# Kernel optimization log

Hardware: AMD Instinct MI355X
Metric: run time of the kernel (lower is better)

The kernel has to match this reference:

```python
import jax, jax.numpy as jnp
import numpy as np

B_SI = 4.1491   # neutron scattering length Si (fm)
B_O = 5.803     # neutron scattering length O (fm)
CUTOFF = 3.5    # tetrahedral neighbour cutoff (A)
BIG = 1e6       # masked-distance sentinel (finite to keep grads NaN-free)


def setup_inputs() -> dict:
    key = jax.random.key(0)
    k1, k2 = jax.random.split(key)
    N, L = 4096, 40.0
    positions = jax.random.uniform(k1, (N, 3), dtype=jnp.float32) * L
    cell = (L * jnp.eye(3)).astype(jnp.float32)
    r_bins = (0.05 + 0.05 * jnp.arange(200, dtype=jnp.float32))      # 0.05..10.0 A
    q_bins = jnp.linspace(0.5, 25.0, 500, dtype=jnp.float32)          # A^-1
    species = jax.random.randint(k2, (N,), 0, 3, dtype=jnp.int32)     # 0=Si, 1/2=O
    return {"positions": positions, "cell": cell, "r_bins": r_bins,
            "q_bins": q_bins, "species": species}


def _pair_geometry(positions, cell):
    # Minimum-image displacements under a general periodic cell.
    disp = positions[:, None, :] - positions[None, :, :]        # [N,N,3]
    frac = disp @ jnp.linalg.inv(cell)
    frac = frac - jnp.round(frac)
    disp = frac @ cell
    d2 = jnp.sum(disp * disp, axis=-1)                           # [N,N]
    self_mask = jnp.eye(positions.shape[0], dtype=bool)
    dist = jnp.sqrt(jnp.where(self_mask, 1.0, d2))               # safe sqrt on diag
    return disp, dist, self_mask


def reference(positions, cell, r_bins, q_bins, species):
    N = positions.shape[0]
    nbins = r_bins.shape[0]
    dtype = positions.dtype

    disp, dist, self_mask = _pair_geometry(positions, cell)

    # --- neutron-weighted G(r): differentiable linear (cloud-in-cell) binning ---
    b = jnp.where(species == 0, B_SI, B_O).astype(dtype)         # per-atom scattering length
    w = (b[:, None] * b[None, :]) / (jnp.mean(b) ** 2)           # Faber-Ziman pair weights
    r0, dr = r_bins[0], r_bins[1] - r_bins[0]
    x = (dist - r0) / dr
    i0 = jnp.floor(x).astype(jnp.int32)
    f = x - i0.astype(dtype)
    valid = (~self_mask) & (i0 >= 0) & (i0 < nbins - 1)
    w0 = jnp.where(valid, w * (1.0 - f), 0.0).ravel()
    w1 = jnp.where(valid, w * f, 0.0).ravel()
    i0f = jnp.clip(i0, 0, nbins - 1).ravel()
    hist = (jnp.zeros(nbins, dtype)
            .at[i0f].add(w0)
            .at[jnp.clip(i0f + 1, 0, nbins - 1)].add(w1))
    V = jnp.abs(jnp.linalg.det(cell))
    rho = N / V
    shell = 4.0 * jnp.pi * r_bins ** 2 * dr                       # ideal-gas shell volume
    G_r = hist / (N * rho * shell)                                # [nbins]

    # --- total correlation function T(r) = 4 pi rho r G(r) ---
    T_r = 4.0 * jnp.pi * rho * r_bins * G_r

    # --- structure factor S(Q) = 1 + 4 pi rho int r^2 (G(r)-1) sinc(Qr) dr ---
    qr = q_bins[:, None] * r_bins[None, :]                        # [nQ, nr]
    integrand = (r_bins ** 2) * (G_r - 1.0)
    S_Q = 1.0 + 4.0 * jnp.pi * rho * dr * jnp.sum(
        integrand[None, :] * jnp.sinc(qr / jnp.pi), axis=1)

    # --- tetrahedral order parameter q_tet over Si centres with O neighbours ---
    central = species == 0
    nbr_ok = (species != 0)[None, :] & (~self_mask)
    nd = jnp.where(nbr_ok, dist, BIG)
    negd, idx = jax.lax.top_k(-nd, 4)                             # 4 nearest O per atom
    d4 = -negd                                                    # [N,4]
    u = jnp.take_along_axis(disp, idx[:, :, None], axis=1) / d4[:, :, None]  # unit vecs
    cosang = jnp.einsum('nkd,nld->nkl', u, u)                     # [N,4,4]
    pair_mask = jnp.triu(jnp.ones((4, 4), bool), 1)               # 6 angle pairs
    q_i = 1.0 - (3.0 / 8.0) * jnp.sum(((cosang + 1.0 / 3.0) ** 2) * pair_mask, axis=(1, 2))
    vf = (central & (d4[:, 3] < CUTOFF)).astype(dtype)            # needs 4 nbrs in cutoff
    q_tet = jnp.sum(q_i * vf) / jnp.maximum(jnp.sum(vf), 1.0)

    return G_r, T_r, S_Q, q_tet
```

## Files before the change

kernel.cpp:

```cpp
#include <hip/hip_runtime.h>
#include <climits>
#include <math.h>


#define B_SI_F 4.1491f
#define B_O_F  5.803f
#define CUTOFF_F 3.5f
#define CS2 12.25350025f
#define NCOPIES 16
#define CAP 32

#define WS_HIST 16
#define WS_ACC  3328
#define WS_CNT  4096

__device__ __forceinline__ bool dless(float da, int ia, float db, int ib) {
    return (da < db) || (da == db && ia < ib);
}

struct CellK {
    float ci0, ci1, ci2, ci3, ci4, ci5, ci6, ci7, ci8;
    float c0, c1, c2, c3, c4, c5, c6, c7, c8;
};

__device__ __forceinline__ CellK make_cell(const float* __restrict__ cellm,
                                           bool& diag) {
    CellK K;
    K.c0 = cellm[0]; K.c1 = cellm[1]; K.c2 = cellm[2];
    K.c3 = cellm[3]; K.c4 = cellm[4]; K.c5 = cellm[5];
    K.c6 = cellm[6]; K.c7 = cellm[7]; K.c8 = cellm[8];
    double m0 = K.c0, m1 = K.c1, m2 = K.c2;
    double m3 = K.c3, m4 = K.c4, m5 = K.c5;
    double m6 = K.c6, m7 = K.c7, m8 = K.c8;
    double det = m0*(m4*m8 - m5*m7) - m1*(m3*m8 - m5*m6) + m2*(m3*m7 - m4*m6);
    double rd = 1.0 / det;
    K.ci0 = (float)( (m4*m8 - m5*m7) * rd);
    K.ci1 = (float)(-(m1*m8 - m2*m7) * rd);
    K.ci2 = (float)( (m1*m5 - m2*m4) * rd);
    K.ci3 = (float)(-(m3*m8 - m5*m6) * rd);
    K.ci4 = (float)( (m0*m8 - m2*m6) * rd);
    K.ci5 = (float)(-(m0*m5 - m2*m3) * rd);
    K.ci6 = (float)( (m3*m7 - m4*m6) * rd);
    K.ci7 = (float)(-(m0*m7 - m1*m6) * rd);
    K.ci8 = (float)( (m0*m4 - m1*m3) * rd);
    diag = (K.c1 == 0.0f) && (K.c2 == 0.0f) && (K.c3 == 0.0f) &&
           (K.c5 == 0.0f) && (K.c6 == 0.0f) && (K.c7 == 0.0f);
    return K;
}

template<bool DIAG>
__device__ __forceinline__ void min_image(const CellK& K,
                                          float dx, float dy, float dz,
                                          float& ex, float& ey, float& ez) {
    if (DIAG) {
        float t0 = dx * K.ci0, t1 = dy * K.ci4, t2 = dz * K.ci8;
        t0 -= rintf(t0);  t1 -= rintf(t1);  t2 -= rintf(t2);
        ex = t0 * K.c0;  ey = t1 * K.c4;  ez = t2 * K.c8;
    } else {
        float f0 = dx*K.ci0 + dy*K.ci3 + dz*K.ci6;
        float f1 = dx*K.ci1 + dy*K.ci4 + dz*K.ci7;
        float f2 = dx*K.ci2 + dy*K.ci5 + dz*K.ci8;
        f0 -= rintf(f0);  f1 -= rintf(f1);  f2 -= rintf(f2);
        ex = f0*K.c0 + f1*K.c3 + f2*K.c6;
        ey = f0*K.c1 + f1*K.c4 + f2*K.c7;
        ez = f0*K.c2 + f1*K.c5 + f2*K.c8;
    }
}

template<bool DIAG>
__device__ __forceinline__ void hist_sweep(const CellK& K,
                                           const float4* __restrict__ sj,
                                           const float4* __restrict__ sjc,
                                           int lbase, int jb0,
                                           float fi0, float fi1, float fi2,
                                           float xi, float yi, float zi,
                                           float wi, float inv_dr, float nrb0,
                                           int nbins_m1, float* shc,
                                           bool iSi, bool iO, bool offdiag, int iidx,
                                           float* __restrict__ cnt,
                                           float4* __restrict__ cand) {
    #pragma unroll 4
    for (int l = 0; l < 64; ++l) {
        const float4 pj = sj[lbase + l];
        float d0 = fi0 - pj.x;  d0 -= rintf(d0);
        float d1 = fi1 - pj.y;  d1 -= rintf(d1);
        float d2 = fi2 - pj.z;  d2 -= rintf(d2);
        float ex, ey, ez;
        if (DIAG) {
            ex = d0 * K.c0;  ey = d1 * K.c4;  ez = d2 * K.c8;
        } else {
            ex = d0*K.c0 + d1*K.c3 + d2*K.c6;
            ey = d0*K.c1 + d1*K.c4 + d2*K.c7;
            ez = d0*K.c2 + d1*K.c5 + d2*K.c8;
        }
        float dsq  = fmaf(ex, ex, fmaf(ey, ey, ez * ez));
        float dist = __builtin_amdgcn_sqrtf(dsq);
        float x  = fmaf(dist, inv_dr, nrb0);
        float fl = floorf(x);
        int   i0 = (int)fl;
        if ((unsigned)i0 < (unsigned)nbins_m1) {
            float w  = wi * pj.w;
            float wf = w * (x - fl);
            atomicAdd(&shc[i0],     w - wf);
            atomicAdd(&shc[i0 + 1], wf);
        }
        if (dsq < CS2) {
            const int jg = jb0 + lbase + l;
            if (iSi && pj.w == B_O_F) {
                float old = atomicAdd(&cnt[iidx], 1.0f);
                int slot = (int)rintf(old);
                if (slot < CAP) {
                    float4 cj = sjc[lbase + l];
                    cj.w = __int_as_float(jg);
                    cand[iidx * CAP + slot] = cj;
                }
            }
            if (offdiag && iO && pj.w == B_SI_F) {
                float old = atomicAdd(&cnt[jg], 1.0f);
                int slot = (int)rintf(old);
                if (slot < CAP)
                    cand[jg * CAP + slot] = make_float4(xi, yi, zi, __int_as_float(iidx));
            }
        }
    }
}

__global__ __launch_bounds__(256) void k_main(const float* __restrict__ cellm,
                                              const float* __restrict__ pos,
                                              const int* __restrict__ species,
                                              const float* __restrict__ rbins,
                                              float* __restrict__ ws,
                                              int N, int nbins, int T) {
    const int tid = threadIdx.x;
    const int bid = blockIdx.x;

    bool diag;
    const CellK K = make_cell(cellm, diag);

    __shared__ float sh[4 * 257];
    __shared__ float sjf[128 * 4];
    __shared__ float sjc[128 * 4];

    for (int u = tid; u < 4 * 257; u += 256) sh[u] = 0.0f;

    int rem = bid, ti = 0;
    while (rem >= T - ti) { rem -= T - ti; ti++; }
    const int tj  = ti + rem;
    const int jb0 = tj * 128;

    for (int u = tid; u < 384; u += 256) {
        int g = 3 * jb0 + u;
        sjc[(u / 3) * 4 + (u % 3)] = (g < 3 * N) ? pos[g] : 0.0f;
    }
    if (tid < 128) {
        int ja = jb0 + tid;
        sjf[tid * 4 + 3] = (ja < N) ? ((species[ja] == 0) ? B_SI_F : B_O_F) : 0.0f;
    }
    __syncthreads();
    if (tid < 128) {
        float x = sjc[tid*4], y = sjc[tid*4+1], z = sjc[tid*4+2];
        float f0, f1, f2;
        if (diag) { f0 = x*K.ci0; f1 = y*K.ci4; f2 = z*K.ci8; }
        else {
            f0 = x*K.ci0 + y*K.ci3 + z*K.ci6;
            f1 = x*K.ci1 + y*K.ci4 + z*K.ci7;
            f2 = x*K.ci2 + y*K.ci5 + z*K.ci8;
        }
        sjf[tid*4] = f0;  sjf[tid*4+1] = f1;  sjf[tid*4+2] = f2;
    }

    const float rb0      = rbins[0];
    const float inv_dr   = 1.0f / (rbins[1] - rbins[0]);
    const float nrb0     = -rb0 * inv_dr;
    const int   nbins_m1 = nbins - 1;

    const int il  = tid & 127;
    const int sub = tid >> 7;
    const int i   = ti * 128 + il;
    const int ig  = min(i, N - 1);
    const float xi = pos[3*ig], yi = pos[3*ig+1], zi = pos[3*ig+2];
    float fi0, fi1, fi2;
    if (diag) { fi0 = xi*K.ci0; fi1 = yi*K.ci4; fi2 = zi*K.ci8; }
    else {
        fi0 = xi*K.ci0 + yi*K.ci3 + zi*K.ci6;
        fi1 = xi*K.ci1 + yi*K.ci4 + zi*K.ci7;
        fi2 = xi*K.ci2 + yi*K.ci5 + zi*K.ci8;
    }
    const int   spi  = species[ig];
    const float b_i  = (spi == 0) ? B_SI_F : B_O_F;
    const float wmul = (ti == tj) ? 1.0f : 2.0f;
    const float wi   = (i < N) ? b_i * wmul : 0.0f;
    const bool iSi = (i < N) && (spi == 0);
    const bool iO  = (i < N) && (spi != 0);
    const bool offdiag = (ti != tj);

    float*  cnt  = ws + WS_CNT;
    float4* cand = (float4*)(ws + WS_CNT + (size_t)N);
    float*  shc  = sh + ((tid >> 4) & 3) * 257;

    __syncthreads();

    const float4* sj   = (const float4*)sjf;
    const float4* sjc4 = (const float4*)sjc;
    const int lbase = sub * 64;
    if (diag) hist_sweep<true >(K, sj, sjc4, lbase, jb0, fi0, fi1, fi2, xi, yi, zi, wi, inv_dr, nrb0, nbins_m1, shc, iSi, iO, offdiag, i, cnt, cand);
    else      hist_sweep<false>(K, sj, sjc4, lbase, jb0, fi0, fi1, fi2, xi, yi, zi, wi, inv_dr, nrb0, nbins_m1, shc, iSi, iO, offdiag, i, cnt, cand);

    __syncthreads();

    float* gh = ws + WS_HIST + (size_t)(bid % NCOPIES) * nbins;
    for (int t = tid; t < nbins; t += 256) {
        float h = sh[t] + sh[257 + t] + sh[514 + t] + sh[771 + t];
        if (h != 0.0f) atomicAdd(&gh[t], h);
    }
}

#define INS4D(c, jc, ex, ey, ez)                                           \
{                                                                          \
    if (dless(c, jc, e3, j3)) {                                            \
        bool lt2 = dless(c, jc, e2, j2);                                   \
        bool lt1 = dless(c, jc, e1, j1);                                   \
        bool lt0 = dless(c, jc, e0, j0);                                   \
        e3 = lt2 ? e2 : c;               j3 = lt2 ? j2 : jc;               \
        x3 = lt2 ? x2 : ex;  y3 = lt2 ? y2 : ey;  z3 = lt2 ? z2 : ez;      \
        e2 = lt2 ? (lt1 ? e1 : c) : e2;  j2 = lt2 ? (lt1 ? j1 : jc) : j2;  \
        x2 = lt2 ? (lt1 ? x1 : ex) : x2;                                   \
        y2 = lt2 ? (lt1 ? y1 : ey) : y2;                                   \
        z2 = lt2 ? (lt1 ? z1 : ez) : z2;                                   \
        e1 = lt1 ? (lt0 ? e0 : c) : e1;  j1 = lt1 ? (lt0 ? j0 : jc) : j1;  \
        x1 = lt1 ? (lt0 ? x0 : ex) : x1;                                   \
        y1 = lt1 ? (lt0 ? y0 : ey) : y1;                                   \
        z1 = lt1 ? (lt0 ? z0 : ez) : z1;                                   \
        e0 = lt0 ? c : e0;               j0 = lt0 ? jc : j0;               \
        x0 = lt0 ? ex : x0;  y0 = lt0 ? ey : y0;  z0 = lt0 ? ez : z0;      \
    }                                                                      \
}

__device__ __forceinline__ float fast_sinc(float x) {
    float rev = x * 0.15915494309189535f;
    rev -= rintf(rev);
    float sn = __builtin_amdgcn_sinf(rev);
    return sn * __builtin_amdgcn_rcpf(x);
}

__global__ __launch_bounds__(256) void k_fin(const float* __restrict__ cellm,
                                             float* __restrict__ ws,
                                             const float* __restrict__ rbins,
                                             const float* __restrict__ qbins,
                                             const int* __restrict__ species,
                                             const float* __restrict__ pos,
                                             float* __restrict__ out,
                                             int N, int nbins, int nq,
                                             int QB, int BT) {
    const int tid = threadIdx.x;
    const int bid = blockIdx.x;

    if (bid >= QB) {
        __shared__ float swq[4], swv[4];
        __shared__ float sacc[128];
        __shared__ int   slast;
        const int tb   = bid - QB;
        const int wid  = tid >> 6;
        const int lane = tid & 63;
        const int s = __builtin_amdgcn_readfirstlane(tb * 4 + wid);

        float* cnt = ws + WS_CNT;
        const float4* cand = (const float4*)(ws + WS_CNT + (size_t)N);

        float qiv = 0.0f, vf = 0.0f;
        if (s < N && species[s] == 0) {
            bool diag;
            const CellK K = make_cell(cellm, diag);
            const float xi = pos[3*s], yi = pos[3*s+1], zi = pos[3*s+2];
            const int c = (int)rintf(cnt[s]);
            if (lane == 0) cnt[s] = 0.0f;

            float e0 = 1e30f, e1 = 1e30f, e2 = 1e30f, e3 = 1e30f;
            int   j0 = INT_MAX, j1 = INT_MAX, j2 = INT_MAX, j3 = INT_MAX;
            float x0 = 0, y0 = 0, z0 = 0, x1 = 0, y1 = 0, z1 = 0;
            float x2 = 0, y2 = 0, z2 = 0, x3 = 0, y3 = 0, z3 = 0;

            if (c <= CAP) {
                if (lane < c) {
                    float4 cd = cand[s * CAP + lane];
                    int j = __float_as_int(cd.w);
                    float ex, ey, ez;
                    if (diag) min_image<true >(K, xi - cd.x, yi - cd.y, zi - cd.z, ex, ey, ez);
                    else      min_image<false>(K, xi - cd.x, yi - cd.y, zi - cd.z, ex, ey, ez);
                    e0 = fmaf(ex, ex, fmaf(ey, ey, ez * ez));
                    j0 = j;  x0 = ex;  y0 = ey;  z0 = ez;
                }
            } else {
                for (int k = lane; k < N; k += 64) {
                    int   sp = species[k];
                    float px = pos[3*k], py = pos[3*k+1], pz = pos[3*k+2];
                    float ex, ey, ez;
                    if (diag) min_image<true >(K, xi - px, yi - py, zi - pz, ex, ey, ez);
                    else      min_image<false>(K, xi - px, yi - py, zi - pz, ex, ey, ez);
                    float d2 = fmaf(ex, ex, fmaf(ey, ey, ez * ez));
                    float cc = (sp != 0 && k != s) ? d2 : 1e30f;
                    int   jc = k;
                    INS4D(cc, jc, ex, ey, ez)
                }
            }

            float r0d, r1d, r2d, r3d;
            int   r0j, r1j, r2j, r3j;
            float rx[4], ry[4], rz[4];
            #define EXTRACT_MIN(RD, RJ, RK)                                    \
            {                                                                  \
                float md = e0; int mj = j0;                                    \
                float mx = x0, my = y0, mz = z0;                               \
                for (int off = 32; off > 0; off >>= 1) {                       \
                    float od = __shfl_xor(md, off, 64);                        \
                    int   oj = __shfl_xor(mj, off, 64);                        \
                    float ox = __shfl_xor(mx, off, 64);                        \
                    float oy = __shfl_xor(my, off, 64);                        \
                    float oz = __shfl_xor(mz, off, 64);                        \
                    bool keep = dless(md, mj, od, oj);                         \
                    md = keep ? md : od;  mj = keep ? mj : oj;                 \
                    mx = keep ? mx : ox;  my = keep ? my : oy;                 \
                    mz = keep ? mz : oz;                                       \
                }                                                              \
                RD = md; RJ = mj; rx[RK] = mx; ry[RK] = my; rz[RK] = mz;       \
                bool pop = (j0 == mj);                                         \
                e0 = pop ? e1 : e0;  j0 = pop ? j1 : j0;                       \
                x0 = pop ? x1 : x0;  y0 = pop ? y1 : y0;  z0 = pop ? z1 : z0;  \
                e1 = pop ? e2 : e1;  j1 = pop ? j2 : j1;                       \
                x1 = pop ? x2 : x1;  y1 = pop ? y2 : y1;  z1 = pop ? z2 : z1;  \
                e2 = pop ? e3 : e2;  j2 = pop ? j3 : j2;                       \
                x2 = pop ? x3 : x2;  y2 = pop ? y3 : y2;  z2 = pop ? z3 : z2;  \
                e3 = pop ? 1e30f : e3;  j3 = pop ? INT_MAX : j3;               \
            }
            EXTRACT_MIN(r0d, r0j, 0)
            EXTRACT_MIN(r1d, r1j, 1)
            EXTRACT_MIN(r2d, r2j, 2)
            EXTRACT_MIN(r3d, r3j, 3)
            #undef EXTRACT_MIN

            if (lane == 0 && r3j != INT_MAX) {
                float dd[4] = {sqrtf(r0d), sqrtf(r1d), sqrtf(r2d), sqrtf(r3d)};
                if (dd[3] < CUTOFF_F) {
                    float ux[4], uy[4], uz[4];
                    #pragma unroll
                    for (int k = 0; k < 4; ++k) {
                        ux[k] = rx[k] / dd[k];
                        uy[k] = ry[k] / dd[k];
                        uz[k] = rz[k] / dd[k];
                    }
                    float s2 = 0.0f;
                    #pragma unroll
                    for (int k = 0; k < 4; ++k)
                        #pragma unroll
                        for (int l = k + 1; l < 4; ++l) {
                            float cs = ux[k]*ux[l] + uy[k]*uy[l] + uz[k]*uz[l];
                            float t  = cs + (1.0f / 3.0f);
                            s2 += t * t;
                        }
                    qiv = 1.0f - 0.375f * s2;
                    vf  = 1.0f;
                }
            }
        }
        if (lane == 0) { swq[wid] = qiv; swv[wid] = vf; }
        __syncthreads();
        if (tid == 0) {
            float bsq = swq[0] + swq[1] + swq[2] + swq[3];
            float bsv = swv[0] + swv[1] + swv[2] + swv[3];
            atomicAdd(&ws[WS_ACC + (tb & 63)], bsq);
            atomicAdd(&ws[WS_ACC + 64 + (tb & 63)], bsv);
            asm volatile("s_waitcnt vmcnt(0)" ::: "memory");
            float old = atomicAdd(&ws[WS_ACC + 128], 1.0f);
            slast = (old > (float)BT - 1.5f) ? 1 : 0;
        }
        __syncthreads();
        if (slast) {
            if (tid < 128) sacc[tid] = atomicAdd(&ws[WS_ACC + tid], 0.0f);
            __syncthreads();
            if (tid == 0) {
                float tq = 0.0f, tv = 0.0f;
                for (int k = 0; k < 64; ++k) { tq += sacc[k]; tv += sacc[64 + k]; }
                out[2 * nbins + nq] = tq / fmaxf(tv, 1.0f);
            }
        }
        return;
    }

    __shared__ float2 srw[256];
    __shared__ int    scnt[256];

    double m0 = cellm[0], m1 = cellm[1], m2 = cellm[2];
    double m3 = cellm[3], m4 = cellm[4], m5 = cellm[5];
    double m6 = cellm[6], m7 = cellm[7], m8 = cellm[8];
    double det = m0*(m4*m8 - m5*m7) - m1*(m3*m8 - m5*m6) + m2*(m3*m7 - m4*m6);
    const float rho = (float)((double)N / fabs(det));

    {
        int c = 0;
        for (int k = tid; k < N; k += 256) c += (species[k] == 0) ? 1 : 0;
        scnt[tid] = c;
    }
    __syncthreads();
    for (int s = 128; s > 0; s >>= 1) {
        if (tid < s) scnt[tid] += scnt[tid + s];
        __syncthreads();
    }
    const int nSi = scnt[0];
    const float mean_b  = ((float)nSi * B_SI_F + (float)(N - nSi) * B_O_F) / (float)N;
    const float w_scale = 1.0f / (mean_b * mean_b);

    const float dr = rbins[1] - rbins[0];
    const float FOURPI = 4.0f * 3.14159265358979323846f;

    for (int t = tid; t < nbins; t += blockDim.x) {
        float h = 0.0f;
        #pragma unroll
        for (int c = 0; c < NCOPIES; ++c) h += ws[WS_HIST + c * nbins + t];
        h *= w_scale;
        float r = rbins[t];
        float shell = FOURPI * r * r * dr;
        float g = h / ((float)N * rho * shell);
        srw[t] = make_float2(r, r * r * (g - 1.0f));
        if (bid == 0) {
            out[t] = g;
            out[nbins + t] = FOURPI * rho * r * g;
        }
    }
    __syncthreads();

    int q = bid * blockDim.x + tid;
    if (q < nq) {
        float qq = qbins[q];
        float s0 = 0.0f, s1 = 0.0f, s2 = 0.0f, s3 = 0.0f;
        int t = 0;
        for (; t + 4 <= nbins; t += 4) {
            float2 a = srw[t], b = srw[t+1], c = srw[t+2], d = srw[t+3];
            s0 += a.y * fast_sinc(qq * a.x);
            s1 += b.y * fast_sinc(qq * b.x);
            s2 += c.y * fast_sinc(qq * c.x);
            s3 += d.y * fast_sinc(qq * d.x);
        }
        for (; t < nbins; ++t) {
            float2 a = srw[t];
            s0 += a.y * fast_sinc(qq * a.x);
        }
        float s = (s0 + s1) + (s2 + s3);
        out[2 * nbins + q] = 1.0f + FOURPI * rho * dr * s;
    }
}

extern "C" void kernel_launch(void* const* d_in, const int* in_sizes, int n_in,
                              void* d_out, int out_size, void* d_ws, size_t ws_size,
                              hipStream_t stream) {
    const float* pos     = (const float*)d_in[0];
    const float* cell    = (const float*)d_in[1];
    const float* rbins   = (const float*)d_in[2];
    const float* qbins   = (const float*)d_in[3];
    const int*   species = (const int*)d_in[4];
    float* out = (float*)d_out;
    float* ws  = (float*)d_ws;

    const int N     = in_sizes[4];
    const int nbins = in_sizes[2];
    const int nq    = in_sizes[3];

    const int T  = (N + 127) / 128;
    const int P  = T * (T + 1) / 2;
    const int BT = (N + 3) / 4;
    const int QB = (nq + 255) / 256;

    k_main<<<P, 256, 0, stream>>>(cell, pos, species, rbins, ws, N, nbins, T);
    k_fin<<<QB + BT, 256, 0, stream>>>(cell, ws, rbins, qbins, species, pos, out, N, nbins, nq, QB, BT);
}
```

Before: 97.71 us.

## Split pair tiles into half-width j blocks, skip far pairs, single shared histogram

Each 128x128 pair tile is now processed by two blocks, each covering 64 j atoms, so twice as many blocks launch and each does half the work. This is meant to improve load balance and CU fill across the GPU. A squared-distance test against the histogram's maximum radius skips the sqrt, floor and binning for pairs outside the binned range. The four padded shared-memory histogram copies become one 256-entry array, which trades possible LDS atomic contention for less shared memory and a cheaper final reduction. The shared histogram zeroing assumes nbins is at most 256.

```diff
diff --git a/kernel.cpp b/kernel.cpp
--- a/kernel.cpp
+++ b/kernel.cpp
@@ -75,12 +75,13 @@
                                            float fi0, float fi1, float fi2,
                                            float xi, float yi, float zi,
                                            float wi, float inv_dr, float nrb0,
-                                           int nbins_m1, float* shc,
+                                           float dmax2, int nbins_m1,
+                                           float* shist,
                                            bool iSi, bool iO, bool offdiag, int iidx,
                                            float* __restrict__ cnt,
                                            float4* __restrict__ cand) {
     #pragma unroll 4
-    for (int l = 0; l < 64; ++l) {
+    for (int l = 0; l < 32; ++l) {
         const float4 pj = sj[lbase + l];
         float d0 = fi0 - pj.x;  d0 -= rintf(d0);
         float d1 = fi1 - pj.y;  d1 -= rintf(d1);
@@ -93,33 +94,35 @@
             ey = d0*K.c1 + d1*K.c4 + d2*K.c7;
             ez = d0*K.c2 + d1*K.c5 + d2*K.c8;
         }
-        float dsq  = fmaf(ex, ex, fmaf(ey, ey, ez * ez));
-        float dist = __builtin_amdgcn_sqrtf(dsq);
-        float x  = fmaf(dist, inv_dr, nrb0);
-        float fl = floorf(x);
-        int   i0 = (int)fl;
-        if ((unsigned)i0 < (unsigned)nbins_m1) {
-            float w  = wi * pj.w;
-            float wf = w * (x - fl);
-            atomicAdd(&shc[i0],     w - wf);
-            atomicAdd(&shc[i0 + 1], wf);
-        }
-        if (dsq < CS2) {
-            const int jg = jb0 + lbase + l;
-            if (iSi && pj.w == B_O_F) {
-                float old = atomicAdd(&cnt[iidx], 1.0f);
-                int slot = (int)rintf(old);
-                if (slot < CAP) {
-                    float4 cj = sjc[lbase + l];
-                    cj.w = __int_as_float(jg);
-                    cand[iidx * CAP + slot] = cj;
+        float dsq = fmaf(ex, ex, fmaf(ey, ey, ez * ez));
+        if (dsq < dmax2) {
+            float dist = __builtin_amdgcn_sqrtf(dsq);
+            float x  = fmaf(dist, inv_dr, nrb0);
+            float fl = floorf(x);
+            int   i0 = (int)fl;
+            if ((unsigned)i0 < (unsigned)nbins_m1) {
+                float w  = wi * pj.w;
+                float wf = w * (x - fl);
+                atomicAdd(&shist[i0],     w - wf);
+                atomicAdd(&shist[i0 + 1], wf);
+            }
+            if (dsq < CS2) {
+                const int jg = jb0 + lbase + l;
+                if (iSi && pj.w == B_O_F) {
+                    float old = atomicAdd(&cnt[iidx], 1.0f);
+                    int slot = (int)rintf(old);
+                    if (slot < CAP) {
+                        float4 cj = sjc[lbase + l];
+                        cj.w = __int_as_float(jg);
+                        cand[iidx * CAP + slot] = cj;
+                    }
                 }
-            }
-            if (offdiag && iO && pj.w == B_SI_F) {
-                float old = atomicAdd(&cnt[jg], 1.0f);
-                int slot = (int)rintf(old);
-                if (slot < CAP)
-                    cand[jg * CAP + slot] = make_float4(xi, yi, zi, __int_as_float(iidx));
+                if (offdiag && iO && pj.w == B_SI_F) {
+                    float old = atomicAdd(&cnt[jg], 1.0f);
+                    int slot = (int)rintf(old);
+                    if (slot < CAP)
+                        cand[jg * CAP + slot] = make_float4(xi, yi, zi, __int_as_float(iidx));
+                }
             }
         }
     }
@@ -137,27 +140,27 @@
     bool diag;
     const CellK K = make_cell(cellm, diag);
 
-    __shared__ float sh[4 * 257];
-    __shared__ float sjf[128 * 4];
-    __shared__ float sjc[128 * 4];
-
-    for (int u = tid; u < 4 * 257; u += 256) sh[u] = 0.0f;
-
-    int rem = bid, ti = 0;
+    __shared__ float shist[256];
+    __shared__ float sjf[64 * 4];
+    __shared__ float sjc[64 * 4];
+    shist[tid] = 0.0f;
+
+    const int jhalf = bid & 1;
+    int rem = bid >> 1, ti = 0;
     while (rem >= T - ti) { rem -= T - ti; ti++; }
     const int tj  = ti + rem;
-    const int jb0 = tj * 128;
-
-    for (int u = tid; u < 384; u += 256) {
-        int g = 3 * jb0 + u;
-        sjc[(u / 3) * 4 + (u % 3)] = (g < 3 * N) ? pos[g] : 0.0f;
-    }
-    if (tid < 128) {
-        int ja = jb0 + tid;
-        sjf[tid * 4 + 3] = (ja < N) ? ((species[ja] == 0) ? B_SI_F : B_O_F) : 0.0f;
+    const int jb0 = tj * 128 + jhalf * 64;
+
+    if (tid < 192) {
+        int g = 3 * jb0 + tid;
+        sjc[(tid / 3) * 4 + (tid % 3)] = (g < 3 * N) ? pos[g] : 0.0f;
+    } else {
+        int a = tid - 192;
+        int ja = jb0 + a;
+        sjf[a * 4 + 3] = (ja < N) ? ((species[ja] == 0) ? B_SI_F : B_O_F) : 0.0f;
     }
     __syncthreads();
-    if (tid < 128) {
+    if (tid < 64) {
         float x = sjc[tid*4], y = sjc[tid*4+1], z = sjc[tid*4+2];
         float f0, f1, f2;
         if (diag) { f0 = x*K.ci0; f1 = y*K.ci4; f2 = z*K.ci8; }
@@ -170,9 +173,12 @@
     }
 
     const float rb0      = rbins[0];
-    const float inv_dr   = 1.0f / (rbins[1] - rbins[0]);
+    const float dr       = rbins[1] - rbins[0];
+    const float inv_dr   = 1.0f / dr;
     const float nrb0     = -rb0 * inv_dr;
     const int   nbins_m1 = nbins - 1;
+    const float dmax     = fmaf((float)nbins_m1, dr, rb0);
+    const float dmax2    = dmax * dmax * 1.000001f;
 
     const int il  = tid & 127;
     const int sub = tid >> 7;
@@ -196,21 +202,20 @@
 
     float*  cnt  = ws + WS_CNT;
     float4* cand = (float4*)(ws + WS_CNT + (size_t)N);
-    float*  shc  = sh + ((tid >> 4) & 3) * 257;
 
     __syncthreads();
 
     const float4* sj   = (const float4*)sjf;
     const float4* sjc4 = (const float4*)sjc;
-    const int lbase = sub * 64;
-    if (diag) hist_sweep<true >(K, sj, sjc4, lbase, jb0, fi0, fi1, fi2, xi, yi, zi, wi, inv_dr, nrb0, nbins_m1, shc, iSi, iO, offdiag, i, cnt, cand);
-    else      hist_sweep<false>(K, sj, sjc4, lbase, jb0, fi0, fi1, fi2, xi, yi, zi, wi, inv_dr, nrb0, nbins_m1, shc, iSi, iO, offdiag, i, cnt, cand);
+    const int lbase = sub * 32;
+    if (diag) hist_sweep<true >(K, sj, sjc4, lbase, jb0, fi0, fi1, fi2, xi, yi, zi, wi, inv_dr, nrb0, dmax2, nbins_m1, shist, iSi, iO, offdiag, i, cnt, cand);
+    else      hist_sweep<false>(K, sj, sjc4, lbase, jb0, fi0, fi1, fi2, xi, yi, zi, wi, inv_dr, nrb0, dmax2, nbins_m1, shist, iSi, iO, offdiag, i, cnt, cand);
 
     __syncthreads();
 
     float* gh = ws + WS_HIST + (size_t)(bid % NCOPIES) * nbins;
     for (int t = tid; t < nbins; t += 256) {
-        float h = sh[t] + sh[257 + t] + sh[514 + t] + sh[771 + t];
+        float h = shist[t];
         if (h != 0.0f) atomicAdd(&gh[t], h);
     }
 }
@@ -465,10 +470,10 @@
     const int nq    = in_sizes[3];
 
     const int T  = (N + 127) / 128;
-    const int P  = T * (T + 1) / 2;
+    const int P2 = T * (T + 1);
     const int BT = (N + 3) / 4;
     const int QB = (nq + 255) / 256;
 
-    k_main<<<P, 256, 0, stream>>>(cell, pos, species, rbins, ws, N, nbins, T);
+    k_main<<<P2, 256, 0, stream>>>(cell, pos, species, rbins, ws, N, nbins, T);
     k_fin<<<QB + BT, 256, 0, stream>>>(cell, ws, rbins, qbins, species, pos, out, N, nbins, nq, QB, BT);
 }
```

New measurement: 93.83 us. 4.0% less time.
